# Kernel tuning notes

Measured on AMD Instinct MI355X. Metric: run time of the kernel, lower is better.

The kernel has to match this reference:

```python
import jax, jax.numpy as jnp
import numpy as np

EPS = 1e-5
NEG_SLOPE = 0.2

def _conv1x1(x, w):
    # x: (B,C,N,K), w: (O,C) -> (B,O,N,K)
    return jnp.einsum('oc,bcnk->bonk', w, x)

def _bn(x, g, b, m, v):
    scale = g / jnp.sqrt(v + EPS)
    return x * scale[None, :, None, None] + (b - m * scale)[None, :, None, None]

def _lrelu(x):
    return jnp.where(x > 0, x, NEG_SLOPE * x)

def setup_inputs() -> dict:
    key = jax.random.key(0)
    specs = {
        'x': ((8, 6, 8192, 20), 'randn'),
        'trans_w': ((64, 6), 'randn'), 'trans_g': ((64,), 'rand'), 'trans_b': ((64,), 'randn'),
        'trans_m': ((64,), 'randn'), 'trans_v': ((64,), 'rand'),
        'pos_w1': ((64, 3), 'randn'), 'pos_g': ((64,), 'rand'), 'pos_b': ((64,), 'randn'),
        'pos_m': ((64,), 'randn'), 'pos_v': ((64,), 'rand'),
        'pos_w2': ((64, 64), 'randn'), 'pos_b2': ((64,), 'randn'),
        'gate_w1': ((16, 6), 'randn'), 'gate_g': ((16,), 'rand'), 'gate_b': ((16,), 'randn'),
        'gate_m': ((16,), 'randn'), 'gate_v': ((16,), 'rand'),
        'gate_w2': ((1, 16), 'randn'), 'gate_b2': ((1,), 'ones'),
        'attn_w1': ((16, 6), 'randn'), 'attn_g': ((16,), 'rand'), 'attn_b': ((16,), 'randn'),
        'attn_m': ((16,), 'randn'), 'attn_v': ((16,), 'rand'),
        'attn_w2': ((64, 16), 'randn'), 'attn_b2': ((64,), 'randn'),
    }
    out = {}
    for i, (name, (shape, fill)) in enumerate(specs.items()):
        k = jax.random.fold_in(key, i)
        if fill == 'randn':
            out[name] = jax.random.normal(k, shape, dtype=jnp.float32) * 0.1
        elif fill == 'rand':
            out[name] = jax.random.uniform(k, shape, dtype=jnp.float32)
        else:  # ones (gate bias init to 2.0 in original; scale ones)
            out[name] = jnp.ones(shape, dtype=jnp.float32) * 2.0
    return out

def reference(x, trans_w, trans_g, trans_b, trans_m, trans_v,
              pos_w1, pos_g, pos_b, pos_m, pos_v, pos_w2, pos_b2,
              gate_w1, gate_g, gate_b, gate_m, gate_v, gate_w2, gate_b2,
              attn_w1, attn_g, attn_b, attn_m, attn_v, attn_w2, attn_b2):
    in_channels = 3
    rel_pos = x[:, in_channels:in_channels + 3, :, :]  # (B,3,N,K)
    # pos_net: conv(3->C) + BN + LReLU + conv(C->C, bias)
    pos_h = _lrelu(_bn(_conv1x1(rel_pos, pos_w1), pos_g, pos_b, pos_m, pos_v))
    pos_enc = _conv1x1(pos_h, pos_w2) + pos_b2[None, :, None, None]
    # trans: conv(2*Cin->C) + BN + LReLU
    trans_feat = _lrelu(_bn(_conv1x1(x, trans_w), trans_g, trans_b, trans_m, trans_v)) + pos_enc
    # gate_net: conv(6->16)+BN+LReLU+conv(16->1,bias)+sigmoid (dropout=0 in eval)
    gate_h = _lrelu(_bn(_conv1x1(x, gate_w1), gate_g, gate_b, gate_m, gate_v))
    gate_map = jax.nn.sigmoid(_conv1x1(gate_h, gate_w2) + gate_b2[None, :, None, None])  # (B,1,N,K)
    clean_feat = trans_feat * gate_map
    # attn_net: conv(6->16)+BN+LReLU+conv(16->C,bias), then + pos_enc, softmax over K
    attn_h = _lrelu(_bn(_conv1x1(x, attn_w1), attn_g, attn_b, attn_m, attn_v))
    attn_logits = _conv1x1(attn_h, attn_w2) + attn_b2[None, :, None, None] + pos_enc
    attn_weights = jax.nn.softmax(attn_logits, axis=-1)
    out_attn = (trans_feat * attn_weights).sum(axis=-1)  # (B,C,N)
    out_max = clean_feat.max(axis=-1)                    # (B,C,N)
    return out_attn + out_max
```

## Files before the change

### kernel.cpp

```cpp
#include <hip/hip_runtime.h>
#include <math.h>

#define NEG 0.2f
#define EPSV 1e-5f

typedef _Float16 v8h __attribute__((ext_vector_type(8)));
typedef _Float16 v4h __attribute__((ext_vector_type(4)));
typedef _Float16 v2h __attribute__((ext_vector_type(2)));
typedef __fp16   f16x2 __attribute__((ext_vector_type(2)));
typedef float    v4f __attribute__((ext_vector_type(4)));

__device__ __forceinline__ float lrelu(float v) { return fmaxf(v, NEG * v); }
__device__ __forceinline__ v4f lrelu4(v4f v) {
    return __builtin_elementwise_max(v, v * NEG);
}
__device__ __forceinline__ v2h lreluh2(v2h v) {
    return __builtin_elementwise_max(v, v * (_Float16)NEG);
}

__device__ __forceinline__ v2h pk(float a, float b) {
    union { f16x2 i; v2h o; } u;
    u.i = __builtin_amdgcn_cvt_pkrtz(a, b);
    return u.o;
}

#define MFMA32(a, b, c) __builtin_amdgcn_mfma_f32_16x16x32_f16((a), (b), (c), 0, 0, 0)
#define MFMA16(a, b, c) __builtin_amdgcn_mfma_f32_16x16x16f16((a), (b), (c), 0, 0, 0)

__global__ __launch_bounds__(256, 3)
void gsl_mfma(const float* __restrict__ x,
              const float* __restrict__ trans_w, const float* __restrict__ trans_g,
              const float* __restrict__ trans_b, const float* __restrict__ trans_m,
              const float* __restrict__ trans_v,
              const float* __restrict__ pos_w1, const float* __restrict__ pos_g,
              const float* __restrict__ pos_b, const float* __restrict__ pos_m,
              const float* __restrict__ pos_v, const float* __restrict__ pos_w2,
              const float* __restrict__ pos_b2,
              const float* __restrict__ gate_w1, const float* __restrict__ gate_g,
              const float* __restrict__ gate_b, const float* __restrict__ gate_m,
              const float* __restrict__ gate_v, const float* __restrict__ gate_w2,
              const float* __restrict__ gate_b2,
              const float* __restrict__ attn_w1, const float* __restrict__ attn_g,
              const float* __restrict__ attn_b, const float* __restrict__ attn_m,
              const float* __restrict__ attn_v, const float* __restrict__ attn_w2,
              const float* __restrict__ attn_b2,
              float* __restrict__ out)
{
    __shared__ _Float16 WH[1920];
    __shared__ float    PB2[64];
    __shared__ _Float16 PHB[4][2][1152];
    __shared__ _Float16 AHB[4][2][320];
    __shared__ _Float16 XSB[4][2560];

    const int tid  = threadIdx.x;
    const int wv   = tid >> 6;
    const int lane = tid & 63;
    const int p    = lane & 15;
    const int q    = lane >> 4;

    const int b  = blockIdx.x >> 7;
    const int n0 = ((blockIdx.x & 127) << 6) | (wv << 4);
    const int n  = n0 | p;

    {
        const float* xw = x + ((size_t)b * 6 * 8192 + n0) * 20;
        _Float16* XS = &XSB[wv][0];
        #pragma unroll
        for (int i = 0; i < 8; ++i) {
            int idx = i * 64 + lane;
            if (idx < 480) {
                int c  = idx / 80;
                int rm = idx - c * 80;
                int pt = rm / 5;
                int k0 = (rm - pt * 5) * 4;
                const float4 v = *(const float4*)(xw + (size_t)c * 163840 + pt * 20 + k0);
                _Float16* dst = XS + pt * 8 + c;
                dst[(k0 + 0) * 128] = (_Float16)v.x;
                dst[(k0 + 1) * 128] = (_Float16)v.y;
                dst[(k0 + 2) * 128] = (_Float16)v.z;
                dst[(k0 + 3) * 128] = (_Float16)v.w;
            }
        }
        #pragma unroll
        for (int i = 0; i < 5; ++i) {
            int idx = i * 64 + lane;
            int k = idx >> 4, pt = idx & 15;
            *(v2h*)(XS + k * 128 + pt * 8 + 6) = (v2h){(_Float16)1.f, (_Float16)0.f};
        }
    }

    if (tid < 64) {
        const int c = tid;
        float sp = pos_g[c] * rsqrtf(pos_v[c] + EPSV);
        float bp = pos_b[c] - pos_m[c] * sp;
        _Float16* row = WH + (c >> 4) * 320 + (c & 15) * 20;
        for (int k = 0; k < 20; ++k) {
            float v = (k >= 3 && k < 6) ? pos_w1[c * 3 + (k - 3)] * sp
                                        : ((k == 6) ? bp : 0.f);
            row[k] = (_Float16)v;
        }
        PB2[c] = pos_b2[c];
    } else if (tid < 80) {
        const int j = tid - 64;
        float sa = attn_g[j] * rsqrtf(attn_v[j] + EPSV);
        float ba = attn_b[j] - attn_m[j] * sa;
        _Float16* row = WH + 1280 + j * 20;
        for (int k = 0; k < 20; ++k)
            row[k] = (_Float16)((k < 6) ? attn_w1[j * 6 + k] * sa
                                        : ((k == 6) ? ba : 0.f));
    } else if (tid < 96) {
        const int j = tid - 80;
        float sg = gate_g[j] * rsqrtf(gate_v[j] + EPSV);
        float bg = gate_b[j] - gate_m[j] * sg;
        _Float16* row = WH + 1600 + j * 20;
        for (int k = 0; k < 20; ++k)
            row[k] = (_Float16)((k < 6) ? gate_w1[j * 6 + k] * sg
                                        : ((k == 6) ? bg : 0.f));
    }

    v8h W2f[4][2];
    v4h WTf[4], WA2f[4];
    #pragma unroll
    for (int mt = 0; mt < 4; ++mt) {
        const int ch = mt * 16 + p;
        #pragma unroll
        for (int h = 0; h < 2; ++h)
            #pragma unroll
            for (int i = 0; i < 8; ++i)
                W2f[mt][h][i] = (_Float16)pos_w2[ch * 64 + h * 32 + q * 8 + i];
        #pragma unroll
        for (int i = 0; i < 4; ++i)
            WA2f[mt][i] = (_Float16)attn_w2[ch * 16 + q * 4 + i];
        float st = trans_g[ch] * rsqrtf(trans_v[ch] + EPSV);
        float bt = trans_b[ch] - trans_m[ch] * st;
        #pragma unroll
        for (int i = 0; i < 4; ++i) {
            int k = q * 4 + i;
            float v = (k < 6) ? trans_w[ch * 6 + k] * st : ((k == 6) ? bt : 0.f);
            WTf[mt][i] = (_Float16)v;
        }
    }
    float g2w[4];
    #pragma unroll
    for (int r = 0; r < 4; ++r) g2w[r] = gate_w2[4 * q + r];
    const float gb2v = gate_b2[0];

    __syncthreads();

    const _Float16* const WP1p = WH + p * 20 + q * 4;
    const _Float16* const WA1p = WH + 1280 + p * 20 + q * 4;
    const _Float16* const WG1p = WH + 1600 + p * 20 + q * 4;
    const float* const    PB2p = PB2 + 4 * q;
    const _Float16* const XS   = &XSB[wv][0];

    _Float16* const PHbase = &PHB[wv][0][0];
    _Float16* const AHbase = &AHB[wv][0][0];

    const int xoff = p * 8 + (q & 1) * 4;

    const v4f zero = {0.f, 0.f, 0.f, 0.f};
    v4f den[4], num[4], cmx[4];
    #pragma unroll
    for (int mt = 0; mt < 4; ++mt) {
        den[mt] = zero; num[mt] = zero;
        cmx[mt] = (v4f){-3.4e38f, -3.4e38f, -3.4e38f, -3.4e38f};
    }

    v4h xv_cur = *(const v4h*)(XS + xoff);
    {
        v4f php[4];
        #pragma unroll
        for (int mt = 0; mt < 4; ++mt)
            php[mt] = MFMA16(*(const v4h*)(WP1p + mt * 320), xv_cur, zero);
        v4f ahp = MFMA16(*(const v4h*)WA1p, xv_cur, zero);
        _Float16* PHW = PHbase + p * 72 + 4 * q;
        #pragma unroll
        for (int mt = 0; mt < 4; ++mt) {
            union { v4h v; v2h h[2]; } u;
            u.h[0] = lreluh2(pk(php[mt][0], php[mt][1]));
            u.h[1] = lreluh2(pk(php[mt][2], php[mt][3]));
            *(v4h*)(PHW + mt * 16) = u.v;
        }
        union { v4h v; v2h h[2]; } ua;
        ua.h[0] = lreluh2(pk(ahp[0], ahp[1]));
        ua.h[1] = lreluh2(pk(ahp[2], ahp[3]));
        *(v4h*)(AHbase + p * 20 + 4 * q) = ua.v;
    }

    #pragma unroll 1
    for (int k = 0; k < 20; ++k) {
        const int sel = k & 1;
        _Float16* PH = PHbase + sel * 1152;
        _Float16* AH = AHbase + sel * 320;
        v8h phf0 = *(const v8h*)(PH + p * 72 + 8 * q);
        v8h phf1 = *(const v8h*)(PH + p * 72 + 32 + 8 * q);
        v4h ahf  = *(const v4h*)(AH + p * 20 + 4 * q);

        v4h xv_nxt = xv_cur;
        if (k < 19) {
            xv_nxt = *(const v4h*)(XS + (k + 1) * 128 + xoff);
            v4f php[4];
            #pragma unroll
            for (int mt = 0; mt < 4; ++mt)
                php[mt] = MFMA16(*(const v4h*)(WP1p + mt * 320), xv_nxt, zero);
            v4f ahp = MFMA16(*(const v4h*)WA1p, xv_nxt, zero);
            _Float16* PHW = PHbase + (sel ^ 1) * 1152 + p * 72 + 4 * q;
            #pragma unroll
            for (int mt = 0; mt < 4; ++mt) {
                union { v4h v; v2h h[2]; } uu;
                uu.h[0] = lreluh2(pk(php[mt][0], php[mt][1]));
                uu.h[1] = lreluh2(pk(php[mt][2], php[mt][3]));
                *(v4h*)(PHW + mt * 16) = uu.v;
            }
            union { v4h v; v2h h[2]; } ua;
            ua.h[0] = lreluh2(pk(ahp[0], ahp[1]));
            ua.h[1] = lreluh2(pk(ahp[2], ahp[3]));
            *(v4h*)(AHbase + (sel ^ 1) * 320 + p * 20 + 4 * q) = ua.v;
        }

        v4f ghp = MFMA16(*(const v4h*)WG1p, xv_cur, zero);
        float ga = 0.f;
        #pragma unroll
        for (int r = 0; r < 4; ++r) ga += g2w[r] * lrelu(ghp[r]);
        ga += __shfl_xor(ga, 16);
        ga += __shfl_xor(ga, 32);
        const float gate = 1.f / (1.f + __expf(-(ga + gb2v)));

        #pragma unroll
        for (int mt = 0; mt < 4; ++mt) {
            v4f pe = MFMA32(W2f[mt][0], phf0, *(const v4f*)(PB2p + mt * 16));
            pe = MFMA32(W2f[mt][1], phf1, pe);
            v4f tfa = MFMA16(WTf[mt], xv_cur, zero);
            v4f tfv = lrelu4(tfa) + pe;
            pe = MFMA16(WA2f[mt], ahf, pe);
            v4f e;
            #pragma unroll
            for (int r = 0; r < 4; ++r) e[r] = __expf(pe[r]);
            den[mt] += e;
            num[mt] += tfv * e;
            cmx[mt] = __builtin_elementwise_max(cmx[mt], tfv * gate);
        }
        xv_cur = xv_nxt;
    }

    #pragma unroll
    for (int mt = 0; mt < 4; ++mt) {
        #pragma unroll
        for (int r = 0; r < 4; ++r) {
            const int ch = mt * 16 + 4 * q + r;
            out[((size_t)(b * 64 + ch)) * 8192 + n] =
                num[mt][r] / den[mt][r] + cmx[mt][r];
        }
    }
}

extern "C" void kernel_launch(void* const* d_in, const int* in_sizes, int n_in,
                              void* d_out, int out_size, void* d_ws, size_t ws_size,
                              hipStream_t stream) {
    const float* x       = (const float*)d_in[0];
    const float* trans_w = (const float*)d_in[1];
    const float* trans_g = (const float*)d_in[2];
    const float* trans_b = (const float*)d_in[3];
    const float* trans_m = (const float*)d_in[4];
    const float* trans_v = (const float*)d_in[5];
    const float* pos_w1  = (const float*)d_in[6];
    const float* pos_g   = (const float*)d_in[7];
    const float* pos_b   = (const float*)d_in[8];
    const float* pos_m   = (const float*)d_in[9];
    const float* pos_v   = (const float*)d_in[10];
    const float* pos_w2  = (const float*)d_in[11];
    const float* pos_b2  = (const float*)d_in[12];
    const float* gate_w1 = (const float*)d_in[13];
    const float* gate_g  = (const float*)d_in[14];
    const float* gate_b  = (const float*)d_in[15];
    const float* gate_m  = (const float*)d_in[16];
    const float* gate_v  = (const float*)d_in[17];
    const float* gate_w2 = (const float*)d_in[18];
    const float* gate_b2 = (const float*)d_in[19];
    const float* attn_w1 = (const float*)d_in[20];
    const float* attn_g  = (const float*)d_in[21];
    const float* attn_b  = (const float*)d_in[22];
    const float* attn_m  = (const float*)d_in[23];
    const float* attn_v  = (const float*)d_in[24];
    const float* attn_w2 = (const float*)d_in[25];
    const float* attn_b2 = (const float*)d_in[26];
    float* out = (float*)d_out;

    gsl_mfma<<<1024, 256, 0, stream>>>(
        x, trans_w, trans_g, trans_b, trans_m, trans_v,
        pos_w1, pos_g, pos_b, pos_m, pos_v, pos_w2, pos_b2,
        gate_w1, gate_g, gate_b, gate_m, gate_v, gate_w2, gate_b2,
        attn_w1, attn_g, attn_b, attn_m, attn_v, attn_w2, attn_b2,
        out);
}
```

Before: 180.4 us.

## Stream x from global per step and move pos_w2 fragments to LDS

Result: no change. 177.0 us (-1.8%).

```diff
diff --git a/kernel.cpp b/kernel.cpp
--- a/kernel.cpp
+++ b/kernel.cpp
@@ -47,10 +47,10 @@
               float* __restrict__ out)
 {
     __shared__ _Float16 WH[1920];
+    __shared__ _Float16 W2L[5120];
     __shared__ float    PB2[64];
     __shared__ _Float16 PHB[4][2][1152];
     __shared__ _Float16 AHB[4][2][320];
-    __shared__ _Float16 XSB[4][2560];
 
     const int tid  = threadIdx.x;
     const int wv   = tid >> 6;
@@ -62,31 +62,15 @@
     const int n0 = ((blockIdx.x & 127) << 6) | (wv << 4);
     const int n  = n0 | p;
 
-    {
-        const float* xw = x + ((size_t)b * 6 * 8192 + n0) * 20;
-        _Float16* XS = &XSB[wv][0];
-        #pragma unroll
-        for (int i = 0; i < 8; ++i) {
-            int idx = i * 64 + lane;
-            if (idx < 480) {
-                int c  = idx / 80;
-                int rm = idx - c * 80;
-                int pt = rm / 5;
-                int k0 = (rm - pt * 5) * 4;
-                const float4 v = *(const float4*)(xw + (size_t)c * 163840 + pt * 20 + k0);
-                _Float16* dst = XS + pt * 8 + c;
-                dst[(k0 + 0) * 128] = (_Float16)v.x;
-                dst[(k0 + 1) * 128] = (_Float16)v.y;
-                dst[(k0 + 2) * 128] = (_Float16)v.z;
-                dst[(k0 + 3) * 128] = (_Float16)v.w;
-            }
-        }
-        #pragma unroll
-        for (int i = 0; i < 5; ++i) {
-            int idx = i * 64 + lane;
-            int k = idx >> 4, pt = idx & 15;
-            *(v2h*)(XS + k * 128 + pt * 8 + 6) = (v2h){(_Float16)1.f, (_Float16)0.f};
-        }
+    #pragma unroll
+    for (int e = 0; e < 16; ++e) {
+        int idx = tid * 16 + e;
+        int t   = idx >> 9;
+        int rem = idx & 511;
+        int pp  = rem >> 5;
+        int ii  = rem & 31;
+        W2L[t * 640 + pp * 40 + ii] =
+            (_Float16)pos_w2[((t >> 1) * 16 + pp) * 64 + (t & 1) * 32 + ii];
     }
 
     if (tid < 64) {
@@ -118,16 +102,10 @@
                                         : ((k == 6) ? bg : 0.f));
     }
 
-    v8h W2f[4][2];
     v4h WTf[4], WA2f[4];
     #pragma unroll
     for (int mt = 0; mt < 4; ++mt) {
         const int ch = mt * 16 + p;
-        #pragma unroll
-        for (int h = 0; h < 2; ++h)
-            #pragma unroll
-            for (int i = 0; i < 8; ++i)
-                W2f[mt][h][i] = (_Float16)pos_w2[ch * 64 + h * 32 + q * 8 + i];
         #pragma unroll
         for (int i = 0; i < 4; ++i)
             WA2f[mt][i] = (_Float16)attn_w2[ch * 16 + q * 4 + i];
@@ -150,13 +128,11 @@
     const _Float16* const WP1p = WH + p * 20 + q * 4;
     const _Float16* const WA1p = WH + 1280 + p * 20 + q * 4;
     const _Float16* const WG1p = WH + 1600 + p * 20 + q * 4;
+    const _Float16* const W2Lp = W2L + p * 40 + q * 8;
     const float* const    PB2p = PB2 + 4 * q;
-    const _Float16* const XS   = &XSB[wv][0];
 
     _Float16* const PHbase = &PHB[wv][0][0];
     _Float16* const AHbase = &AHB[wv][0][0];
-
-    const int xoff = p * 8 + (q & 1) * 4;
 
     const v4f zero = {0.f, 0.f, 0.f, 0.f};
     v4f den[4], num[4], cmx[4];
@@ -166,7 +142,23 @@
         cmx[mt] = (v4f){-3.4e38f, -3.4e38f, -3.4e38f, -3.4e38f};
     }
 
-    v4h xv_cur = *(const v4h*)(XS + xoff);
+    const float* xb = x + ((size_t)(b * 6) * 8192 + n) * 20;
+    const int hi = q & 1;
+
+    float nx[6];
+    #pragma unroll
+    for (int c = 0; c < 6; ++c) nx[c] = xb[(size_t)c * 163840];
+
+    v4h xv_cur;
+    {
+        float s0 = hi ? nx[4] : nx[0], s1 = hi ? nx[5] : nx[1];
+        float s2 = hi ? 1.f : nx[2],   s3 = hi ? 0.f : nx[3];
+        v2h lo = pk(s0, s1), hh = pk(s2, s3);
+        xv_cur = (v4h){lo.x, lo.y, hh.x, hh.y};
+    }
+    #pragma unroll
+    for (int c = 0; c < 6; ++c) nx[c] = xb[(size_t)c * 163840 + 1];
+
     {
         v4f php[4];
         #pragma unroll
@@ -189,6 +181,8 @@
 
     #pragma unroll 1
     for (int k = 0; k < 20; ++k) {
+        asm volatile("" ::: "memory");
+
         const int sel = k & 1;
         _Float16* PH = PHbase + sel * 1152;
         _Float16* AH = AHbase + sel * 320;
@@ -198,7 +192,14 @@
 
         v4h xv_nxt = xv_cur;
         if (k < 19) {
-            xv_nxt = *(const v4h*)(XS + (k + 1) * 128 + xoff);
+            float s0 = hi ? nx[4] : nx[0], s1 = hi ? nx[5] : nx[1];
+            float s2 = hi ? 1.f : nx[2],   s3 = hi ? 0.f : nx[3];
+            v2h lo = pk(s0, s1), hh = pk(s2, s3);
+            xv_nxt = (v4h){lo.x, lo.y, hh.x, hh.y};
+            const int kn = (k < 18) ? k + 2 : 19;
+            #pragma unroll
+            for (int c = 0; c < 6; ++c) nx[c] = xb[(size_t)c * 163840 + kn];
+
             v4f php[4];
             #pragma unroll
             for (int mt = 0; mt < 4; ++mt)
@@ -228,8 +229,10 @@
 
         #pragma unroll
         for (int mt = 0; mt < 4; ++mt) {
-            v4f pe = MFMA32(W2f[mt][0], phf0, *(const v4f*)(PB2p + mt * 16));
-            pe = MFMA32(W2f[mt][1], phf1, pe);
+            v8h w2a = *(const v8h*)(W2Lp + (mt * 2 + 0) * 640);
+            v8h w2b = *(const v8h*)(W2Lp + (mt * 2 + 1) * 640);
+            v4f pe = MFMA32(w2a, phf0, *(const v4f*)(PB2p + mt * 16));
+            pe = MFMA32(w2b, phf1, pe);
             v4f tfa = MFMA16(WTf[mt], xv_cur, zero);
             v4f tfv = lrelu4(tfa) + pe;
             pe = MFMA16(WA2f[mt], ahf, pe);
```

## Keep hidden activations in registers via MFMA output-as-input layout, drop LDS staging

Applied to the files above, without the earlier changes.

Measured after the change: 186.4 us. 3.3% more time.

```diff
diff --git a/kernel.cpp b/kernel.cpp
--- a/kernel.cpp
+++ b/kernel.cpp
@@ -4,7 +4,6 @@
 #define NEG 0.2f
 #define EPSV 1e-5f
 
-typedef _Float16 v8h __attribute__((ext_vector_type(8)));
 typedef _Float16 v4h __attribute__((ext_vector_type(4)));
 typedef _Float16 v2h __attribute__((ext_vector_type(2)));
 typedef __fp16   f16x2 __attribute__((ext_vector_type(2)));
@@ -14,17 +13,18 @@
 __device__ __forceinline__ v4f lrelu4(v4f v) {
     return __builtin_elementwise_max(v, v * NEG);
 }
-__device__ __forceinline__ v2h lreluh2(v2h v) {
-    return __builtin_elementwise_max(v, v * (_Float16)NEG);
-}
 
 __device__ __forceinline__ v2h pk(float a, float b) {
     union { f16x2 i; v2h o; } u;
     u.i = __builtin_amdgcn_cvt_pkrtz(a, b);
     return u.o;
 }
-
-#define MFMA32(a, b, c) __builtin_amdgcn_mfma_f32_16x16x32_f16((a), (b), (c), 0, 0, 0)
+__device__ __forceinline__ v4h pack4l(v4f v) {
+    v = lrelu4(v);
+    v2h a = pk(v[0], v[1]), b = pk(v[2], v[3]);
+    return (v4h){a.x, a.y, b.x, b.y};
+}
+
 #define MFMA16(a, b, c) __builtin_amdgcn_mfma_f32_16x16x16f16((a), (b), (c), 0, 0, 0)
 
 __global__ __launch_bounds__(256, 3)
@@ -46,10 +46,7 @@
               const float* __restrict__ attn_b2,
               float* __restrict__ out)
 {
-    __shared__ _Float16 WH[1920];
     __shared__ float    PB2[64];
-    __shared__ _Float16 PHB[4][2][1152];
-    __shared__ _Float16 AHB[4][2][320];
     __shared__ _Float16 XSB[4][2560];
 
     const int tid  = threadIdx.x;
@@ -88,46 +85,17 @@
             *(v2h*)(XS + k * 128 + pt * 8 + 6) = (v2h){(_Float16)1.f, (_Float16)0.f};
         }
     }
-
-    if (tid < 64) {
-        const int c = tid;
-        float sp = pos_g[c] * rsqrtf(pos_v[c] + EPSV);
-        float bp = pos_b[c] - pos_m[c] * sp;
-        _Float16* row = WH + (c >> 4) * 320 + (c & 15) * 20;
-        for (int k = 0; k < 20; ++k) {
-            float v = (k >= 3 && k < 6) ? pos_w1[c * 3 + (k - 3)] * sp
-                                        : ((k == 6) ? bp : 0.f);
-            row[k] = (_Float16)v;
-        }
-        PB2[c] = pos_b2[c];
-    } else if (tid < 80) {
-        const int j = tid - 64;
-        float sa = attn_g[j] * rsqrtf(attn_v[j] + EPSV);
-        float ba = attn_b[j] - attn_m[j] * sa;
-        _Float16* row = WH + 1280 + j * 20;
-        for (int k = 0; k < 20; ++k)
-            row[k] = (_Float16)((k < 6) ? attn_w1[j * 6 + k] * sa
-                                        : ((k == 6) ? ba : 0.f));
-    } else if (tid < 96) {
-        const int j = tid - 80;
-        float sg = gate_g[j] * rsqrtf(gate_v[j] + EPSV);
-        float bg = gate_b[j] - gate_m[j] * sg;
-        _Float16* row = WH + 1600 + j * 20;
-        for (int k = 0; k < 20; ++k)
-            row[k] = (_Float16)((k < 6) ? gate_w1[j * 6 + k] * sg
-                                        : ((k == 6) ? bg : 0.f));
-    }
-
-    v8h W2f[4][2];
-    v4h WTf[4], WA2f[4];
+    if (tid < 64) PB2[tid] = pos_b2[tid];
+
+    v4h W2f[4][4], WTf[4], WA2f[4], WP1f[4], WA1f, WG1f;
     #pragma unroll
     for (int mt = 0; mt < 4; ++mt) {
         const int ch = mt * 16 + p;
         #pragma unroll
-        for (int h = 0; h < 2; ++h)
+        for (int kb = 0; kb < 4; ++kb)
             #pragma unroll
-            for (int i = 0; i < 8; ++i)
-                W2f[mt][h][i] = (_Float16)pos_w2[ch * 64 + h * 32 + q * 8 + i];
+            for (int i = 0; i < 4; ++i)
+                W2f[mt][kb][i] = (_Float16)pos_w2[ch * 64 + kb * 16 + q * 4 + i];
         #pragma unroll
         for (int i = 0; i < 4; ++i)
             WA2f[mt][i] = (_Float16)attn_w2[ch * 16 + q * 4 + i];
@@ -139,6 +107,33 @@
             float v = (k < 6) ? trans_w[ch * 6 + k] * st : ((k == 6) ? bt : 0.f);
             WTf[mt][i] = (_Float16)v;
         }
+        float sp = pos_g[ch] * rsqrtf(pos_v[ch] + EPSV);
+        float bp = pos_b[ch] - pos_m[ch] * sp;
+        #pragma unroll
+        for (int i = 0; i < 4; ++i) {
+            int k = q * 4 + i;
+            float v = (k >= 3 && k < 6) ? pos_w1[ch * 3 + (k - 3)] * sp
+                                        : ((k == 6) ? bp : 0.f);
+            WP1f[mt][i] = (_Float16)v;
+        }
+    }
+    {
+        float sa = attn_g[p] * rsqrtf(attn_v[p] + EPSV);
+        float ba = attn_b[p] - attn_m[p] * sa;
+        #pragma unroll
+        for (int i = 0; i < 4; ++i) {
+            int k = q * 4 + i;
+            WA1f[i] = (_Float16)((k < 6) ? attn_w1[p * 6 + k] * sa
+                                         : ((k == 6) ? ba : 0.f));
+        }
+        float sg = gate_g[p] * rsqrtf(gate_v[p] + EPSV);
+        float bg = gate_b[p] - gate_m[p] * sg;
+        #pragma unroll
+        for (int i = 0; i < 4; ++i) {
+            int k = q * 4 + i;
+            WG1f[i] = (_Float16)((k < 6) ? gate_w1[p * 6 + k] * sg
+                                         : ((k == 6) ? bg : 0.f));
+        }
     }
     float g2w[4];
     #pragma unroll
@@ -147,15 +142,8 @@
 
     __syncthreads();
 
-    const _Float16* const WP1p = WH + p * 20 + q * 4;
-    const _Float16* const WA1p = WH + 1280 + p * 20 + q * 4;
-    const _Float16* const WG1p = WH + 1600 + p * 20 + q * 4;
     const float* const    PB2p = PB2 + 4 * q;
     const _Float16* const XS   = &XSB[wv][0];
-
-    _Float16* const PHbase = &PHB[wv][0][0];
-    _Float16* const AHbase = &AHB[wv][0][0];
-
     const int xoff = p * 8 + (q & 1) * 4;
 
     const v4f zero = {0.f, 0.f, 0.f, 0.f};
@@ -166,59 +154,16 @@
         cmx[mt] = (v4f){-3.4e38f, -3.4e38f, -3.4e38f, -3.4e38f};
     }
 
-    v4h xv_cur = *(const v4h*)(XS + xoff);
-    {
-        v4f php[4];
-        #pragma unroll
-        for (int mt = 0; mt < 4; ++mt)
-            php[mt] = MFMA16(*(const v4h*)(WP1p + mt * 320), xv_cur, zero);
-        v4f ahp = MFMA16(*(const v4h*)WA1p, xv_cur, zero);
-        _Float16* PHW = PHbase + p * 72 + 4 * q;
-        #pragma unroll
-        for (int mt = 0; mt < 4; ++mt) {
-            union { v4h v; v2h h[2]; } u;
-            u.h[0] = lreluh2(pk(php[mt][0], php[mt][1]));
-            u.h[1] = lreluh2(pk(php[mt][2], php[mt][3]));
-            *(v4h*)(PHW + mt * 16) = u.v;
-        }
-        union { v4h v; v2h h[2]; } ua;
-        ua.h[0] = lreluh2(pk(ahp[0], ahp[1]));
-        ua.h[1] = lreluh2(pk(ahp[2], ahp[3]));
-        *(v4h*)(AHbase + p * 20 + 4 * q) = ua.v;
-    }
-
     #pragma unroll 1
     for (int k = 0; k < 20; ++k) {
-        const int sel = k & 1;
-        _Float16* PH = PHbase + sel * 1152;
-        _Float16* AH = AHbase + sel * 320;
-        v8h phf0 = *(const v8h*)(PH + p * 72 + 8 * q);
-        v8h phf1 = *(const v8h*)(PH + p * 72 + 32 + 8 * q);
-        v4h ahf  = *(const v4h*)(AH + p * 20 + 4 * q);
-
-        v4h xv_nxt = xv_cur;
-        if (k < 19) {
-            xv_nxt = *(const v4h*)(XS + (k + 1) * 128 + xoff);
-            v4f php[4];
-            #pragma unroll
-            for (int mt = 0; mt < 4; ++mt)
-                php[mt] = MFMA16(*(const v4h*)(WP1p + mt * 320), xv_nxt, zero);
-            v4f ahp = MFMA16(*(const v4h*)WA1p, xv_nxt, zero);
-            _Float16* PHW = PHbase + (sel ^ 1) * 1152 + p * 72 + 4 * q;
-            #pragma unroll
-            for (int mt = 0; mt < 4; ++mt) {
-                union { v4h v; v2h h[2]; } uu;
-                uu.h[0] = lreluh2(pk(php[mt][0], php[mt][1]));
-                uu.h[1] = lreluh2(pk(php[mt][2], php[mt][3]));
-                *(v4h*)(PHW + mt * 16) = uu.v;
-            }
-            union { v4h v; v2h h[2]; } ua;
-            ua.h[0] = lreluh2(pk(ahp[0], ahp[1]));
-            ua.h[1] = lreluh2(pk(ahp[2], ahp[3]));
-            *(v4h*)(AHbase + (sel ^ 1) * 320 + p * 20 + 4 * q) = ua.v;
-        }
-
-        v4f ghp = MFMA16(*(const v4h*)WG1p, xv_cur, zero);
+        const v4h xv = *(const v4h*)(XS + k * 128 + xoff);
+
+        v4f php[4];
+        #pragma unroll
+        for (int kb = 0; kb < 4; ++kb) php[kb] = MFMA16(WP1f[kb], xv, zero);
+        v4f ahp = MFMA16(WA1f, xv, zero);
+        v4f ghp = MFMA16(WG1f, xv, zero);
+
         float ga = 0.f;
         #pragma unroll
         for (int r = 0; r < 4; ++r) ga += g2w[r] * lrelu(ghp[r]);
@@ -226,11 +171,18 @@
         ga += __shfl_xor(ga, 32);
         const float gate = 1.f / (1.f + __expf(-(ga + gb2v)));
 
+        v4h phb[4];
+        #pragma unroll
+        for (int kb = 0; kb < 4; ++kb) phb[kb] = pack4l(php[kb]);
+        const v4h ahf = pack4l(ahp);
+
         #pragma unroll
         for (int mt = 0; mt < 4; ++mt) {
-            v4f pe = MFMA32(W2f[mt][0], phf0, *(const v4f*)(PB2p + mt * 16));
-            pe = MFMA32(W2f[mt][1], phf1, pe);
-            v4f tfa = MFMA16(WTf[mt], xv_cur, zero);
+            v4f pe = *(const v4f*)(PB2p + mt * 16);
+            #pragma unroll
+            for (int kb = 0; kb < 4; ++kb)
+                pe = MFMA16(W2f[mt][kb], phb[kb], pe);
+            v4f tfa = MFMA16(WTf[mt], xv, zero);
             v4f tfv = lrelu4(tfa) + pe;
             pe = MFMA16(WA2f[mt], ahf, pe);
             v4f e;
@@ -240,7 +192,6 @@
             num[mt] += tfv * e;
             cmx[mt] = __builtin_elementwise_max(cmx[mt], tfv * gate);
         }
-        xv_cur = xv_nxt;
     }
 
     #pragma unroll
```
